# Optimization experiments

Hardware: AMD Instinct MI355X
Metric: run time of the kernel (lower is better)

## Reference

```python
import jax, jax.numpy as jnp
import numpy as np

B, V = 4, 10242
N = B * V            # 40968 packed vertices
E_PER = 30720        # edges per mesh
HID = 128


def _bilinear_sample(fm, grid):
    """pytorch3d vert_align core: grid_sample(align_corners=True, bilinear).
    fm: [B,C,H,W], grid: [B,V,2] xy in [-1,1] -> [B,V,C]."""
    b_, c_, h_, w_ = fm.shape
    x = (grid[..., 0] + 1.0) * 0.5 * (w_ - 1)
    y = (grid[..., 1] + 1.0) * 0.5 * (h_ - 1)
    x0f, y0f = jnp.floor(x), jnp.floor(y)
    wx1, wy1 = x - x0f, y - y0f
    wx0, wy0 = 1.0 - wx1, 1.0 - wy1
    x0 = jnp.clip(x0f, 0, w_ - 1).astype(jnp.int32)
    x1 = jnp.clip(x0f + 1, 0, w_ - 1).astype(jnp.int32)
    y0 = jnp.clip(y0f, 0, h_ - 1).astype(jnp.int32)
    y1 = jnp.clip(y0f + 1, 0, h_ - 1).astype(jnp.int32)
    fmt = jnp.transpose(fm, (0, 2, 3, 1))  # [B,H,W,C]
    bi = jnp.arange(b_)[:, None]
    g = lambda yy, xx: fmt[bi, yy, xx]     # [B,V,C]
    return ((wy0 * wx0)[..., None] * g(y0, x0)
            + (wy0 * wx1)[..., None] * g(y0, x1)
            + (wy1 * wx0)[..., None] * g(y1, x0)
            + (wy1 * wx1)[..., None] * g(y1, x1))


def _graph_conv(x, edges, w0, b0, w1, b1):
    """pytorch3d GraphConv (undirected): W0 x_i + sum over both edge dirs of W1 x_j."""
    h0 = x @ w0 + b0
    h1 = x @ w1 + b1
    e0, e1 = edges[:, 0], edges[:, 1]
    agg = jnp.zeros_like(h0).at[e0].add(h1[e1]).at[e1].add(h1[e0])
    return h0 + agg


def setup_inputs() -> dict:
    key = jax.random.key(0)
    ks = jax.random.split(key, 20)
    s = 0.05
    # per-mesh edges, offset into packed index space
    e = jax.random.randint(ks[0], (B, E_PER, 2), 0, V)
    e = e + (jnp.arange(B) * V)[:, None, None]
    return {
        "feat1": jax.random.normal(ks[1], (B, 256, 56, 56), jnp.float32),
        "feat2": jax.random.normal(ks[2], (B, 512, 28, 28), jnp.float32),
        "feat3": jax.random.normal(ks[3], (B, 1024, 14, 14), jnp.float32),
        "feat4": jax.random.normal(ks[4], (B, 2048, 7, 7), jnp.float32),
        "aligned_verts": jax.random.uniform(ks[5], (B, V, 3), jnp.float32, -1.0, 1.0),
        "verts_packed": jax.random.normal(ks[6], (N, 3), jnp.float32),
        "image_enc": jax.random.normal(ks[7], (B, 256), jnp.float32),
        "edges": e.reshape(B * E_PER, 2).astype(jnp.int64),
        "bottleneck_w": jax.random.normal(ks[8], (3840, HID), jnp.float32) * s,
        "bottleneck_b": jnp.zeros((HID,), jnp.float32),
        "g0_w0": jax.random.normal(ks[9], (387, HID), jnp.float32) * s,
        "g0_b0": jnp.zeros((HID,), jnp.float32),
        "g0_w1": jax.random.normal(ks[10], (387, HID), jnp.float32) * s,
        "g0_b1": jnp.zeros((HID,), jnp.float32),
        "gw0": jax.random.normal(ks[11], (7, HID, HID), jnp.float32) * s,
        "gb0": jnp.zeros((7, HID), jnp.float32),
        "gw1": jax.random.normal(ks[12], (7, HID, HID), jnp.float32) * s,
        "gb1": jnp.zeros((7, HID), jnp.float32),
        "off_w": jax.random.normal(ks[13], (HID, 3), jnp.float32) * s,
        "off_b": jnp.zeros((3,), jnp.float32),
    }


def reference(feat1, feat2, feat3, feat4, aligned_verts, verts_packed, image_enc,
              edges, bottleneck_w, bottleneck_b, g0_w0, g0_b0, g0_w1, g0_b1,
              gw0, gb0, gw1, gb1, off_w, off_b):
    grid = aligned_verts[..., :2]  # vert_align uses xy only
    samp = jnp.concatenate([_bilinear_sample(f, grid)
                            for f in (feat1, feat2, feat3, feat4)], axis=-1)
    samp = samp.reshape(N, 3840)  # return_packed=True
    vfeat = jax.nn.relu(samp @ bottleneck_w + bottleneck_b)
    enc = jnp.repeat(image_enc, V, axis=0)  # repeat_interleave
    x = jnp.concatenate([vfeat, verts_packed, enc], axis=1)  # [N,387]
    x = jax.nn.relu(_graph_conv(x, edges, g0_w0, g0_b0, g0_w1, g0_b1))
    for i in range(7):
        x = jax.nn.relu(_graph_conv(x, edges, gw0[i], gb0[i], gw1[i], gb1[i]))
    return x @ off_w + off_b  # delta_v [N,3]
```

## Files before the change

### kernel.cpp

```cpp
#include <hip/hip_runtime.h>

static inline int ceil_div(int a, int b) { return (a + b - 1) / b; }

typedef __attribute__((ext_vector_type(8))) short short8;
typedef __attribute__((ext_vector_type(4))) float floatx4;

__device__ __forceinline__ unsigned short f2bf(float f) {
    unsigned int u = __float_as_uint(f);
    unsigned int r = (u + 0x7fffu + ((u >> 16) & 1u)) >> 16;
    return (unsigned short)r;
}
__device__ __forceinline__ float bf2f(unsigned short h) {
    return __uint_as_float(((unsigned int)h) << 16);
}

__global__ __launch_bounds__(1024) void scan1_k(const int* __restrict__ deg,
                                                int* __restrict__ excl,
                                                int* __restrict__ bsum, int Nv) {
    __shared__ int s[1024];
    int tid = threadIdx.x;
    int i = blockIdx.x * 1024 + tid;
    int v = (i < Nv) ? deg[i] : 0;
    s[tid] = v;
    __syncthreads();
    for (int off = 1; off < 1024; off <<= 1) {
        int t = (tid >= off) ? s[tid - off] : 0;
        __syncthreads();
        if (tid >= off) s[tid] += t;
        __syncthreads();
    }
    if (i < Nv) excl[i] = s[tid] - v;
    if (tid == 1023) bsum[blockIdx.x] = s[1023];
}

__global__ __launch_bounds__(64) void scan2_k(int* __restrict__ bsum, int nb) {
    __shared__ int s[64];
    int tid = threadIdx.x;
    int v = (tid < nb) ? bsum[tid] : 0;
    s[tid] = v;
    __syncthreads();
    for (int off = 1; off < 64; off <<= 1) {
        int t = (tid >= off) ? s[tid - off] : 0;
        __syncthreads();
        if (tid >= off) s[tid] += t;
        __syncthreads();
    }
    if (tid < nb) bsum[tid] = s[tid] - v;
}

__global__ __launch_bounds__(1024) void scan3_k(const int* __restrict__ excl,
                                                const int* __restrict__ bsum,
                                                const int* __restrict__ deg,
                                                int* __restrict__ rowptr,
                                                int* __restrict__ cursor, int Nv) {
    int i = blockIdx.x * 1024 + threadIdx.x;
    if (i < Nv) {
        int val = excl[i] + bsum[blockIdx.x];
        rowptr[i] = val;
        cursor[i] = val;
        if (i == Nv - 1) rowptr[Nv] = val + deg[i];
    }
}

__global__ __launch_bounds__(256) void fill_adj_k(const int* __restrict__ edges,
                                                  int* __restrict__ cursor,
                                                  int* __restrict__ adj, int E) {
    int e = blockIdx.x * blockDim.x + threadIdx.x;
    if (e < E) {
        int a = edges[2 * e], b = edges[2 * e + 1];
        adj[atomicAdd(&cursor[a], 1)] = b;
        adj[atomicAdd(&cursor[b], 1)] = a;
    }
}

__global__ __launch_bounds__(256) void fatpre_k(const int* __restrict__ edges,
                                                int* __restrict__ deg, int E, int nE,
                                                const float* __restrict__ g0w0,
                                                const float* __restrict__ g0w1,
                                                const float* __restrict__ gw0,
                                                const float* __restrict__ gw1,
                                                unsigned short* __restrict__ Wt,
                                                const float* __restrict__ bw,
                                                unsigned short* __restrict__ bwT,
                                                const float* __restrict__ enc,
                                                float* __restrict__ encp, int B_) {
    int bid = blockIdx.x;
    int tid = threadIdx.x;
    if (bid < nE) {
        int e = bid * 256 + tid;
        if (e < E) {
            atomicAdd(&deg[edges[2 * e]], 1);
            atomicAdd(&deg[edges[2 * e + 1]], 1);
        }
    } else if (bid < nE + 16) {
        int lh = bid - nE;
        int l = lh >> 1, h = lh & 1;
        const float* src;
        if (l == 0) src = h ? g0w1 : g0w0;
        else src = (h ? gw1 : gw0) + (size_t)(l - 1) * 16384;
        unsigned short* dst = Wt + (size_t)lh * 16384;
        for (int idx = tid; idx < 16384; idx += 256) {
            int n = idx >> 7, k = idx & 127;
            dst[n * 128 + k] = f2bf(src[k * 128 + n]);
        }
    } else if (bid < nE + 46) {
        int blk = bid - nE - 16;
        for (int idx = tid; idx < 16384; idx += 256) {
            int n = idx >> 7, kk = idx & 127;
            bwT[(size_t)n * 3840 + blk * 128 + kk] =
                f2bf(bw[(size_t)(blk * 128 + kk) * 128 + n]);
        }
    } else {
        int b = bid - nE - 46;
        int sH = tid >> 7;
        int j = tid & 127;
        const float* w = sH ? g0w1 : g0w0;
        const float* eb = enc + b * 256;
        float acc = 0.f;
        for (int c = 0; c < 256; ++c) acc = fmaf(eb[c], w[(131 + c) * 128 + j], acc);
        encp[(sH * B_ + b) * 128 + j] = acc;
    }
}

__global__ __launch_bounds__(256) void proj_all_k(
    const float* __restrict__ fm1, const float* __restrict__ fm2,
    const float* __restrict__ fm3, const float* __restrict__ fm4,
    const unsigned short* __restrict__ bwT, float* __restrict__ o1, float* __restrict__ o2,
    float* __restrict__ o3, float* __restrict__ o4, int B_) {
    __shared__ unsigned short wlds[8192];

    int tid = threadIdx.x;
    int n1 = 49 * B_ * 2, n2 = 13 * B_ * 4, n3 = 4 * B_ * 8;
    int bid = blockIdx.x;
    const float* fm;
    float* op;
    int C, HW, PT, idx, koff;
    if (bid < n1) {
        fm = fm1; op = o1; C = 256; HW = 3136; PT = 49; idx = bid; koff = 0;
    } else if (bid < n1 + n2) {
        fm = fm2; op = o2; C = 512; HW = 784; PT = 13; idx = bid - n1; koff = 256;
    } else if (bid < n1 + n2 + n3) {
        fm = fm3; op = o3; C = 1024; HW = 196; PT = 4; idx = bid - n1 - n2; koff = 768;
    } else {
        fm = fm4; op = o4; C = 2048; HW = 49; PT = 1; idx = bid - n1 - n2 - n3; koff = 1792;
    }
    int pt = idx % PT;
    int r2 = idx / PT;
    int b = r2 % B_;
    int zz = r2 / B_;
    int p0 = pt * 64;
    const float* fmb = fm + (size_t)b * C * HW;
    int kcf0 = zz * 128;

    int wave = tid >> 6, lane = tid & 63;
    int row16 = lane & 15, quad = lane >> 4;
    int p = p0 + wave * 16 + row16;
    bool pok = (p < HW);
    int pc = pok ? p : 0;

    floatx4 acc[8];
#pragma unroll
    for (int j = 0; j < 8; ++j) acc[j] = (floatx4){0.f, 0.f, 0.f, 0.f};

#pragma unroll
    for (int zz2 = 0; zz2 < 2; ++zz2) {
        int kcf = kcf0 + zz2 * 64;
        int kcw = koff + kcf;
        if (zz2) __syncthreads();
#pragma unroll
        for (int l = 0; l < 4; ++l) {
            int i2 = tid + l * 256;
            int n = i2 >> 3, c16 = i2 & 7;
            *(short8*)&wlds[n * 64 + ((c16 ^ (n & 7)) * 8)] =
                *(const short8*)(bwT + (size_t)n * 3840 + kcw + c16 * 8);
        }
        short8 ax[2];
#pragma unroll
        for (int ks = 0; ks < 2; ++ks) {
#pragma unroll
            for (int j = 0; j < 8; ++j) {
                float v = pok ? fmb[(size_t)(kcf + ks * 32 + quad * 8 + j) * HW + pc] : 0.f;
                ax[ks][j] = (short)f2bf(v);
            }
        }
        __syncthreads();
#pragma unroll
        for (int ks = 0; ks < 2; ++ks) {
            int c = ks * 4 + quad;
#pragma unroll
            for (int nt = 0; nt < 8; ++nt) {
                int wr = nt * 16 + row16;
                short8 bwf = *(short8*)&wlds[wr * 64 + ((c ^ (wr & 7)) * 8)];
                acc[nt] =
                    __builtin_amdgcn_mfma_f32_16x16x32_bf16(ax[ks], bwf, acc[nt], 0, 0, 0);
            }
        }
    }

    float* obase = op + (size_t)b * HW * 128;
#pragma unroll
    for (int nt = 0; nt < 8; ++nt) {
        int colg = nt * 16 + row16;
#pragma unroll
        for (int rr = 0; rr < 4; ++rr) {
            int pr = p0 + wave * 16 + quad * 4 + rr;
            if (pr < HW) atomicAdd(&obase[(size_t)pr * 128 + colg], acc[nt][rr]);
        }
    }
}

__device__ __forceinline__ float sample_level(const float* __restrict__ pp, int Hh, int Ww,
                                              float gx, float gy, int j) {
    float x = (gx + 1.f) * 0.5f * (float)(Ww - 1);
    float y = (gy + 1.f) * 0.5f * (float)(Hh - 1);
    float x0f = floorf(x), y0f = floorf(y);
    float wx1 = x - x0f, wy1 = y - y0f;
    float wx0 = 1.f - wx1, wy0 = 1.f - wy1;
    int x0 = (int)fminf(fmaxf(x0f, 0.f), (float)(Ww - 1));
    int x1 = (int)fminf(fmaxf(x0f + 1.f, 0.f), (float)(Ww - 1));
    int y0 = (int)fminf(fmaxf(y0f, 0.f), (float)(Hh - 1));
    int y1 = (int)fminf(fmaxf(y0f + 1.f, 0.f), (float)(Hh - 1));
    const float* r00 = pp + (size_t)(y0 * Ww + x0) * 128;
    const float* r01 = pp + (size_t)(y0 * Ww + x1) * 128;
    const float* r10 = pp + (size_t)(y1 * Ww + x0) * 128;
    const float* r11 = pp + (size_t)(y1 * Ww + x1) * 128;
    return wy0 * (wx0 * r00[j] + wx1 * r01[j]) + wy1 * (wx0 * r10[j] + wx1 * r11[j]);
}

__global__ __launch_bounds__(128) void sample_bottleneck_k(
    const float* __restrict__ av, const float* __restrict__ pp1, const float* __restrict__ pp2,
    const float* __restrict__ pp3, const float* __restrict__ pp4, const float* __restrict__ bb,
    const float* __restrict__ verts, const float* __restrict__ encp,
    const float* __restrict__ g0w0, const float* __restrict__ g0w1,
    const float* __restrict__ g0b0, const float* __restrict__ g0b1,
    unsigned short* __restrict__ X, unsigned short* __restrict__ H, int V_, int B_) {
    int n = blockIdx.x, j = threadIdx.x;
    int b = n / V_;
    float gx = av[(size_t)n * 3 + 0];
    float gy = av[(size_t)n * 3 + 1];
    float acc = bb[j];
    acc += sample_level(pp1 + (size_t)b * 3136 * 128, 56, 56, gx, gy, j);
    acc += sample_level(pp2 + (size_t)b * 784 * 128, 28, 28, gx, gy, j);
    acc += sample_level(pp3 + (size_t)b * 196 * 128, 14, 14, gx, gy, j);
    acc += sample_level(pp4 + (size_t)b * 49 * 128, 7, 7, gx, gy, j);
    X[(size_t)n * 128 + j] = f2bf(fmaxf(acc, 0.f));
    float v0 = verts[n * 3 + 0], v1 = verts[n * 3 + 1], v2 = verts[n * 3 + 2];
    float h0 = encp[(0 * B_ + b) * 128 + j] + g0b0[j] + v0 * g0w0[128 * 128 + j] +
               v1 * g0w0[129 * 128 + j] + v2 * g0w0[130 * 128 + j];
    float h1 = encp[(1 * B_ + b) * 128 + j] + g0b1[j] + v0 * g0w1[128 * 128 + j] +
               v1 * g0w1[129 * 128 + j] + v2 * g0w1[130 * 128 + j];
    H[(size_t)n * 256 + j] = f2bf(h0);
    H[(size_t)n * 256 + 128 + j] = f2bf(h1);
}

__global__ __launch_bounds__(256) void agg0_k(const unsigned short* __restrict__ X,
                                              const unsigned short* __restrict__ H,
                                              const int* __restrict__ rowptr,
                                              const int* __restrict__ adj,
                                              unsigned short* __restrict__ AggX,
                                              unsigned short* __restrict__ AggH, int Nv) {
    int wave = threadIdx.x >> 6, lane = threadIdx.x & 63;
    int n0 = (blockIdx.x * 4 + wave) * 2;
    if (n0 >= Nv) return;
    const unsigned int* Xu = (const unsigned int*)X;
    int r0 = rowptr[n0], r1 = rowptr[n0 + 1], r2 = rowptr[n0 + 2];
    float a0 = 0.f, a1 = 0.f, b0 = 0.f, b1 = 0.f;
    float c0 = 0.f, c1 = 0.f, d0 = 0.f, d1 = 0.f;
    int tA = r0, tB = r1;
    while (tA < r1 || tB < r2) {
        int nbA[8], nbB[8];
        unsigned int wA[8], wB[8], hA[8], hB[8];
#pragma unroll
        for (int q = 0; q < 8; ++q) {
            int ia = tA + q; ia = (ia < r1) ? ia : (r1 - 1); ia = (ia < 0) ? 0 : ia;
            nbA[q] = adj[ia];
            int ib = tB + q; ib = (ib < r2) ? ib : (r2 - 1); ib = (ib < 0) ? 0 : ib;
            nbB[q] = adj[ib];
        }
#pragma unroll
        for (int q = 0; q < 8; ++q) {
            wA[q] = Xu[(size_t)nbA[q] * 64 + lane];
            wB[q] = Xu[(size_t)nbB[q] * 64 + lane];
            hA[q] = *(const unsigned int*)(H + (size_t)nbA[q] * 256 + 128 + 2 * lane);
            hB[q] = *(const unsigned int*)(H + (size_t)nbB[q] * 256 + 128 + 2 * lane);
        }
#pragma unroll
        for (int q = 0; q < 8; ++q) {
            if (tA + q < r1) {
                a0 += bf2f((unsigned short)(wA[q] & 0xffff));
                a1 += bf2f((unsigned short)(wA[q] >> 16));
                c0 += bf2f((unsigned short)(hA[q] & 0xffff));
                c1 += bf2f((unsigned short)(hA[q] >> 16));
            }
            if (tB + q < r2) {
                b0 += bf2f((unsigned short)(wB[q] & 0xffff));
                b1 += bf2f((unsigned short)(wB[q] >> 16));
                d0 += bf2f((unsigned short)(hB[q] & 0xffff));
                d1 += bf2f((unsigned short)(hB[q] >> 16));
            }
        }
        tA += 8;
        tB += 8;
    }
    *(unsigned int*)(AggX + (size_t)n0 * 128 + 2 * lane) =
        (unsigned int)f2bf(a0) | ((unsigned int)f2bf(a1) << 16);
    *(unsigned int*)(AggX + (size_t)(n0 + 1) * 128 + 2 * lane) =
        (unsigned int)f2bf(b0) | ((unsigned int)f2bf(b1) << 16);
    *(unsigned int*)(AggH + (size_t)n0 * 128 + 2 * lane) =
        (unsigned int)f2bf(c0) | ((unsigned int)f2bf(c1) << 16);
    *(unsigned int*)(AggH + (size_t)(n0 + 1) * 128 + 2 * lane) =
        (unsigned int)f2bf(d0) | ((unsigned int)f2bf(d1) << 16);
}

__global__ __launch_bounds__(256) void agg_x_k(const unsigned short* __restrict__ X,
                                               const int* __restrict__ rowptr,
                                               const int* __restrict__ adj,
                                               unsigned short* __restrict__ Agg, int Nv,
                                               int Etot) {
    int wave = threadIdx.x >> 6, lane = threadIdx.x & 63;
    int n0 = (blockIdx.x * 4 + wave) * 4;
    if (n0 >= Nv) return;
    int g = lane >> 4, c = lane & 15;
    int rp = rowptr[min(n0 + (lane & 7), Nv)];
    int sg = __shfl(rp, g);
    int eg = __shfl(rp, g + 1);
    int m = eg - sg;
    m = max(m, __shfl_xor(m, 16));
    m = max(m, __shfl_xor(m, 32));

    float acc[8];
#pragma unroll
    for (int j = 0; j < 8; ++j) acc[j] = 0.f;

    for (int it = 0; it < m; it += 8) {
        int t = sg + it + (lane & 7);
        int adjv = adj[min(t, Etot - 1)];
        short8 buf[8];
#pragma unroll
        for (int q = 0; q < 8; ++q) {
            int nbq = __shfl(adjv, (lane & 48) + q);
            buf[q] = *(const short8*)(X + (size_t)nbq * 128 + c * 8);
        }
#pragma unroll
        for (int q = 0; q < 8; ++q) {
            bool ok = (sg + it + q < eg);
#pragma unroll
            for (int j = 0; j < 8; ++j) {
                float v = bf2f((unsigned short)buf[q][j]);
                acc[j] += ok ? v : 0.f;
            }
        }
    }

    if (n0 + g < Nv) {
        short8 o;
#pragma unroll
        for (int j = 0; j < 8; ++j) o[j] = (short)f2bf(acc[j]);
        *(short8*)(Agg + (size_t)(n0 + g) * 128 + c * 8) = o;
    }
}

__global__ __launch_bounds__(256, 3) void gemm_dual_k(
    const unsigned short* __restrict__ Xin, const unsigned short* __restrict__ Agg,
    const unsigned short* __restrict__ Wt,
    const float* __restrict__ b0, const float* __restrict__ b1,
    const unsigned short* __restrict__ h0b, const unsigned short* __restrict__ aggh,
    const int* __restrict__ degv, unsigned short* __restrict__ Xout, int M) {
    __shared__ unsigned short wlds[16384];
    __shared__ unsigned short cs[64 * 72];
    __shared__ float bS[128];

    int tid = threadIdx.x;
    int m0 = blockIdx.x * 128;
    int yb = blockIdx.y;

    int wave = tid >> 6, lane = tid & 63;
    int row16 = lane & 15;
    int quad = lane >> 4;
    int wrow = wave * 16;

    short8 axT[2][4], agT[2][4];
    int dgT[2][4];
    {
        int g = min(m0 + wrow + row16, M - 1);
#pragma unroll
        for (int ks = 0; ks < 4; ++ks) {
            int koff = ks * 32 + quad * 8;
            axT[0][ks] = *(const short8*)(Xin + (size_t)g * 128 + koff);
            agT[0][ks] = *(const short8*)(Agg + (size_t)g * 128 + koff);
        }
#pragma unroll
        for (int rr = 0; rr < 4; ++rr)
            dgT[0][rr] = degv[min(m0 + wrow + quad * 4 + rr, M - 1)];
    }

    if (tid < 64) {
        bS[tid] = b0 ? b0[yb * 64 + tid] : 0.f;
        bS[64 + tid] = b1 ? b1[yb * 64 + tid] : 0.f;
    }

    const unsigned short* W0h = Wt + (size_t)yb * 64 * 128;
    const unsigned short* W1h = Wt + 16384 + (size_t)yb * 64 * 128;
#pragma unroll
    for (int l = 0; l < 8; ++l) {
        int idx = tid + l * 256;
        int half = idx >> 10;
        int r = (idx >> 4) & 63;
        int c16 = idx & 15;
        int sw = (c16 ^ (r & 15)) * 8;
        const unsigned short* src = (half ? W1h : W0h) + r * 128 + c16 * 8;
        *(short8*)&wlds[half * 8192 + r * 128 + sw] = *(const short8*)src;
    }
    __syncthreads();

    {
        int g = min(m0 + 64 + wrow + row16, M - 1);
#pragma unroll
        for (int ks = 0; ks < 4; ++ks) {
            int koff = ks * 32 + quad * 8;
            axT[1][ks] = *(const short8*)(Xin + (size_t)g * 128 + koff);
            agT[1][ks] = *(const short8*)(Agg + (size_t)g * 128 + koff);
        }
#pragma unroll
        for (int rr = 0; rr < 4; ++rr)
            dgT[1][rr] = degv[min(m0 + 64 + wrow + quad * 4 + rr, M - 1)];
    }

#pragma unroll
    for (int t = 0; t < 2; ++t) {
        int mT = m0 + t * 64;
        floatx4 acc[4];
#pragma unroll
        for (int j = 0; j < 4; j++) acc[j] = (floatx4){0.f, 0.f, 0.f, 0.f};

#pragma unroll
        for (int ks = 0; ks < 4; ++ks) {
            int c = ks * 4 + quad;
#pragma unroll
            for (int nt = 0; nt < 4; ++nt) {
                int wr = nt * 16 + row16;
                short8 bw0 = *(short8*)&wlds[wr * 128 + ((c ^ row16) * 8)];
                short8 bw1 = *(short8*)&wlds[8192 + wr * 128 + ((c ^ row16) * 8)];
                acc[nt] = __builtin_amdgcn_mfma_f32_16x16x32_bf16(axT[t][ks], bw0, acc[nt], 0, 0, 0);
                acc[nt] = __builtin_amdgcn_mfma_f32_16x16x32_bf16(agT[t][ks], bw1, acc[nt], 0, 0, 0);
            }
        }

#pragma unroll
        for (int nt = 0; nt < 4; ++nt) {
            int colh = nt * 16 + row16;
            int colg = yb * 64 + colh;
            float bc0 = bS[colh];
            float bc1 = bS[64 + colh];
#pragma unroll
            for (int rr = 0; rr < 4; ++rr) {
                int row = wrow + quad * 4 + rr;
                int gm = mT + row;
                float v = acc[nt][rr] + bc0 + (float)dgT[t][rr] * bc1;
                if (h0b && gm < M)
                    v += bf2f(h0b[(size_t)gm * 256 + colg]) +
                         bf2f(aggh[(size_t)gm * 128 + colg]);
                cs[row * 72 + colh] = f2bf(fmaxf(v, 0.f));
            }
        }
        __syncthreads();

        {
            int r = tid >> 2;
            int cq = (tid & 3) * 16;
            int gm = mT + r;
            if (gm < M) {
                unsigned short* dst = Xout + (size_t)gm * 128 + yb * 64 + cq;
                *(short8*)dst = *(short8*)&cs[r * 72 + cq];
                *(short8*)(dst + 8) = *(short8*)&cs[r * 72 + cq + 8];
            }
        }
        __syncthreads();
    }
}

__global__ __launch_bounds__(256) void head_k(const unsigned short* __restrict__ X,
                                              const float* __restrict__ off_w,
                                              const float* __restrict__ off_b,
                                              float* __restrict__ out, int Nv) {
    int wave = threadIdx.x >> 6, lane = threadIdx.x & 63;
    int n = blockIdx.x * 4 + wave;
    if (n >= Nv) return;
    unsigned int u = *(const unsigned int*)(X + (size_t)n * 128 + 2 * lane);
    float x0 = bf2f((unsigned short)(u & 0xffff));
    float x1 = bf2f((unsigned short)(u >> 16));
    int c0 = 2 * lane, c1 = 2 * lane + 1;
    float p0 = x0 * off_w[c0 * 3 + 0] + x1 * off_w[c1 * 3 + 0];
    float p1 = x0 * off_w[c0 * 3 + 1] + x1 * off_w[c1 * 3 + 1];
    float p2 = x0 * off_w[c0 * 3 + 2] + x1 * off_w[c1 * 3 + 2];
#pragma unroll
    for (int m = 1; m < 64; m <<= 1) {
        p0 += __shfl_xor(p0, m);
        p1 += __shfl_xor(p1, m);
        p2 += __shfl_xor(p2, m);
    }
    if (lane == 0) {
        out[n * 3 + 0] = p0 + off_b[0];
        out[n * 3 + 1] = p1 + off_b[1];
        out[n * 3 + 2] = p2 + off_b[2];
    }
}

extern "C" void kernel_launch(void* const* d_in, const int* in_sizes, int n_in, void* d_out,
                              int out_size, void* d_ws, size_t ws_size, hipStream_t stream) {
    const float* feat1 = (const float*)d_in[0];
    const float* feat2 = (const float*)d_in[1];
    const float* feat3 = (const float*)d_in[2];
    const float* feat4 = (const float*)d_in[3];
    const float* av = (const float*)d_in[4];
    const float* verts = (const float*)d_in[5];
    const float* image_enc = (const float*)d_in[6];
    const int* edges = (const int*)d_in[7];
    const float* bw = (const float*)d_in[8];
    const float* bb = (const float*)d_in[9];
    const float* g0w0 = (const float*)d_in[10];
    const float* g0b0 = (const float*)d_in[11];
    const float* g0w1 = (const float*)d_in[12];
    const float* g0b1 = (const float*)d_in[13];
    const float* gw0 = (const float*)d_in[14];
    const float* gb0 = (const float*)d_in[15];
    const float* gw1 = (const float*)d_in[16];
    const float* gb1 = (const float*)d_in[17];
    const float* off_w = (const float*)d_in[18];
    const float* off_b = (const float*)d_in[19];

    int B_ = in_sizes[6] / 256;
    int N_ = in_sizes[5] / 3;
    int V_ = N_ / B_;
    int E_ = in_sizes[7] / 2;

    char* wsb = (char*)d_ws;
    size_t off = 0;
    auto alloc = [&](size_t bytes) -> void* {
        void* p = (void*)(wsb + off);
        off += (bytes + 255) & ~(size_t)255;
        return p;
    };
    int S1 = B_ * 3136 * 128;
    int S2 = B_ * 784 * 128;
    int S3 = B_ * 196 * 128;
    int S4 = B_ * 49 * 128;
    float* pp1 = (float*)alloc((size_t)S1 * 4);
    float* pp2 = (float*)alloc((size_t)S2 * 4);
    float* pp3 = (float*)alloc((size_t)S3 * 4);
    float* pp4 = (float*)alloc((size_t)S4 * 4);
    size_t pp_bytes = off;
    unsigned short* XA = (unsigned short*)alloc((size_t)N_ * 128 * 2);
    unsigned short* XB = (unsigned short*)alloc((size_t)N_ * 128 * 2);
    unsigned short* AggB = (unsigned short*)alloc((size_t)N_ * 128 * 2);
    unsigned short* AggH = (unsigned short*)alloc((size_t)N_ * 128 * 2);
    unsigned short* Hb = (unsigned short*)alloc((size_t)N_ * 256 * 2);
    unsigned short* Wt = (unsigned short*)alloc((size_t)8 * 2 * 128 * 128 * 2);
    unsigned short* bwT = (unsigned short*)alloc((size_t)128 * 3840 * 2);
    float* encp = (float*)alloc((size_t)2 * B_ * 128 * 4);
    int* deg = (int*)alloc((size_t)(N_ + 1) * 4);
    int* rowptr = (int*)alloc((size_t)(N_ + 1) * 4);
    int* cursor = (int*)alloc((size_t)N_ * 4);
    int* excl = (int*)alloc((size_t)N_ * 4);
    int* bsum = (int*)alloc((size_t)64 * 4);
    int* adj = (int*)alloc((size_t)2 * E_ * 4);

    hipMemsetAsync(deg, 0, (N_ + 1) * sizeof(int), stream);
    hipMemsetAsync(wsb, 0, pp_bytes, stream);

    int nE = ceil_div(E_, 256);
    fatpre_k<<<nE + 46 + B_, 256, 0, stream>>>(edges, deg, E_, nE, g0w0, g0w1, gw0, gw1, Wt,
                                               bw, bwT, image_enc, encp, B_);

    int nb = ceil_div(N_, 1024);
    scan1_k<<<nb, 1024, 0, stream>>>(deg, excl, bsum, N_);
    scan2_k<<<1, 64, 0, stream>>>(bsum, nb);
    scan3_k<<<nb, 1024, 0, stream>>>(excl, bsum, deg, rowptr, cursor, N_);
    fill_adj_k<<<ceil_div(E_, 256), 256, 0, stream>>>(edges, cursor, adj, E_);

    int nproj = 49 * B_ * 2 + 13 * B_ * 4 + 4 * B_ * 8 + 1 * B_ * 16;
    proj_all_k<<<nproj, 256, 0, stream>>>(feat1, feat2, feat3, feat4, bwT, pp1, pp2, pp3, pp4,
                                          B_);

    sample_bottleneck_k<<<N_, 128, 0, stream>>>(av, pp1, pp2, pp3, pp4, bb, verts, encp, g0w0,
                                                g0w1, g0b0, g0b1, XA, Hb, V_, B_);

    dim3 ggrid(ceil_div(N_, 128), 2);
    agg0_k<<<ceil_div(N_, 8), 256, 0, stream>>>(XA, Hb, rowptr, adj, AggB, AggH, N_);
    gemm_dual_k<<<ggrid, 256, 0, stream>>>(XA, AggB, Wt, nullptr, nullptr, Hb, AggH, deg, XB,
                                           N_);
    unsigned short* Xc = XB;
    unsigned short* Xn = XA;
    int agrid4 = ceil_div(N_, 16);
    for (int i = 0; i < 7; ++i) {
        agg_x_k<<<agrid4, 256, 0, stream>>>(Xc, rowptr, adj, AggB, N_, 2 * E_);
        gemm_dual_k<<<ggrid, 256, 0, stream>>>(Xc, AggB, Wt + (size_t)(i + 1) * 32768,
                                               gb0 + i * 128, gb1 + i * 128, nullptr, nullptr,
                                               deg, Xn, N_);
        unsigned short* t = Xc;
        Xc = Xn;
        Xn = t;
    }
    head_k<<<ceil_div(N_, 4), 256, 0, stream>>>(Xc, off_w, off_b, (float*)d_out, N_);
}
```

Measured before the change: 428.4 us.

## Fuse head into last GEMM, merge scan stages, vectorize layer-0 aggregation

Removes the separate scan2 kernel by having each scan3 block compute its own prefix offset with a wave reduction. Rewrites agg0 to the agg_x layout: four nodes per wave, 16 lanes per node, short8 vector gathers. It also folds the self h0 term into AggH, so the GEMM epilogue no longer reads h0b. The final output head is fused into the last GEMM epilogue using shuffle reductions and atomicAdd into a zeroed output. This saves launches and one activation round-trip, but adds float atomics whose accumulation order is nondeterministic.

After: 431.4 us, median of 2. Within noise of the previous version (+0.7%).

```diff
diff --git a/kernel.cpp b/kernel.cpp
--- a/kernel.cpp
+++ b/kernel.cpp
@@ -33,29 +33,22 @@
     if (tid == 1023) bsum[blockIdx.x] = s[1023];
 }
 
-__global__ __launch_bounds__(64) void scan2_k(int* __restrict__ bsum, int nb) {
-    __shared__ int s[64];
-    int tid = threadIdx.x;
-    int v = (tid < nb) ? bsum[tid] : 0;
-    s[tid] = v;
-    __syncthreads();
-    for (int off = 1; off < 64; off <<= 1) {
-        int t = (tid >= off) ? s[tid - off] : 0;
-        __syncthreads();
-        if (tid >= off) s[tid] += t;
-        __syncthreads();
-    }
-    if (tid < nb) bsum[tid] = s[tid] - v;
-}
-
 __global__ __launch_bounds__(1024) void scan3_k(const int* __restrict__ excl,
                                                 const int* __restrict__ bsum,
                                                 const int* __restrict__ deg,
                                                 int* __restrict__ rowptr,
-                                                int* __restrict__ cursor, int Nv) {
+                                                int* __restrict__ cursor, int Nv, int nb) {
+    __shared__ int offS;
+    if (threadIdx.x < 64) {
+        int v = (threadIdx.x < min((int)blockIdx.x, nb)) ? bsum[threadIdx.x] : 0;
+#pragma unroll
+        for (int m = 1; m < 64; m <<= 1) v += __shfl_xor(v, m);
+        if (threadIdx.x == 0) offS = v;
+    }
+    __syncthreads();
     int i = blockIdx.x * 1024 + threadIdx.x;
     if (i < Nv) {
-        int val = excl[i] + bsum[blockIdx.x];
+        int val = excl[i] + offS;
         rowptr[i] = val;
         cursor[i] = val;
         if (i == Nv - 1) rowptr[Nv] = val + deg[i];
@@ -258,58 +251,60 @@
                                               const int* __restrict__ rowptr,
                                               const int* __restrict__ adj,
                                               unsigned short* __restrict__ AggX,
-                                              unsigned short* __restrict__ AggH, int Nv) {
+                                              unsigned short* __restrict__ AggH, int Nv,
+                                              int Etot) {
     int wave = threadIdx.x >> 6, lane = threadIdx.x & 63;
-    int n0 = (blockIdx.x * 4 + wave) * 2;
+    int n0 = (blockIdx.x * 4 + wave) * 4;
     if (n0 >= Nv) return;
-    const unsigned int* Xu = (const unsigned int*)X;
-    int r0 = rowptr[n0], r1 = rowptr[n0 + 1], r2 = rowptr[n0 + 2];
-    float a0 = 0.f, a1 = 0.f, b0 = 0.f, b1 = 0.f;
-    float c0 = 0.f, c1 = 0.f, d0 = 0.f, d1 = 0.f;
-    int tA = r0, tB = r1;
-    while (tA < r1 || tB < r2) {
-        int nbA[8], nbB[8];
-        unsigned int wA[8], wB[8], hA[8], hB[8];
+    int g = lane >> 4, c = lane & 15;
+    int rp = rowptr[min(n0 + (lane & 7), Nv)];
+    int sg = __shfl(rp, g);
+    int eg = __shfl(rp, g + 1);
+    int m = eg - sg;
+    m = max(m, __shfl_xor(m, 16));
+    m = max(m, __shfl_xor(m, 32));
+
+    int n = n0 + g;
+    bool nok = (n < Nv);
+    int nc = nok ? n : (Nv - 1);
+    float accx[8], acch[8];
+    short8 h0v = *(const short8*)(H + (size_t)nc * 256 + c * 8);
+#pragma unroll
+    for (int j = 0; j < 8; ++j) {
+        accx[j] = 0.f;
+        acch[j] = bf2f((unsigned short)h0v[j]);
+    }
+
+    for (int it = 0; it < m; it += 8) {
+        int t = sg + it + (lane & 7);
+        int adjv = adj[min(t, Etot - 1)];
+        short8 bx[8], bh[8];
 #pragma unroll
         for (int q = 0; q < 8; ++q) {
-            int ia = tA + q; ia = (ia < r1) ? ia : (r1 - 1); ia = (ia < 0) ? 0 : ia;
-            nbA[q] = adj[ia];
-            int ib = tB + q; ib = (ib < r2) ? ib : (r2 - 1); ib = (ib < 0) ? 0 : ib;
-            nbB[q] = adj[ib];
+            int nbq = __shfl(adjv, (lane & 48) + q);
+            bx[q] = *(const short8*)(X + (size_t)nbq * 128 + c * 8);
+            bh[q] = *(const short8*)(H + (size_t)nbq * 256 + 128 + c * 8);
         }
 #pragma unroll
         for (int q = 0; q < 8; ++q) {
-            wA[q] = Xu[(size_t)nbA[q] * 64 + lane];
-            wB[q] = Xu[(size_t)nbB[q] * 64 + lane];
-            hA[q] = *(const unsigned int*)(H + (size_t)nbA[q] * 256 + 128 + 2 * lane);
-            hB[q] = *(const unsigned int*)(H + (size_t)nbB[q] * 256 + 128 + 2 * lane);
-        }
-#pragma unroll
-        for (int q = 0; q < 8; ++q) {
-            if (tA + q < r1) {
-                a0 += bf2f((unsigned short)(wA[q] & 0xffff));
-                a1 += bf2f((unsigned short)(wA[q] >> 16));
-                c0 += bf2f((unsigned short)(hA[q] & 0xffff));
-                c1 += bf2f((unsigned short)(hA[q] >> 16));
-            }
-            if (tB + q < r2) {
-                b0 += bf2f((unsigned short)(wB[q] & 0xffff));
-                b1 += bf2f((unsigned short)(wB[q] >> 16));
-                d0 += bf2f((unsigned short)(hB[q] & 0xffff));
-                d1 += bf2f((unsigned short)(hB[q] >> 16));
-            }
-        }
-        tA += 8;
-        tB += 8;
-    }
-    *(unsigned int*)(AggX + (size_t)n0 * 128 + 2 * lane) =
-        (unsigned int)f2bf(a0) | ((unsigned int)f2bf(a1) << 16);
-    *(unsigned int*)(AggX + (size_t)(n0 + 1) * 128 + 2 * lane) =
-        (unsigned int)f2bf(b0) | ((unsigned int)f2bf(b1) << 16);
-    *(unsigned int*)(AggH + (size_t)n0 * 128 + 2 * lane) =
-        (unsigned int)f2bf(c0) | ((unsigned int)f2bf(c1) << 16);
-    *(unsigned int*)(AggH + (size_t)(n0 + 1) * 128 + 2 * lane) =
-        (unsigned int)f2bf(d0) | ((unsigned int)f2bf(d1) << 16);
+            bool ok = (sg + it + q < eg);
+#pragma unroll
+            for (int j = 0; j < 8; ++j) {
+                accx[j] += ok ? bf2f((unsigned short)bx[q][j]) : 0.f;
+                acch[j] += ok ? bf2f((unsigned short)bh[q][j]) : 0.f;
+            }
+        }
+    }
+    if (nok) {
+        short8 ox, oh;
+#pragma unroll
+        for (int j = 0; j < 8; ++j) {
+            ox[j] = (short)f2bf(accx[j]);
+            oh[j] = (short)f2bf(acch[j]);
+        }
+        *(short8*)(AggX + (size_t)n * 128 + c * 8) = ox;
+        *(short8*)(AggH + (size_t)n * 128 + c * 8) = oh;
+    }
 }
 
 __global__ __launch_bounds__(256) void agg_x_k(const unsigned short* __restrict__ X,
@@ -364,11 +359,13 @@
     const unsigned short* __restrict__ Xin, const unsigned short* __restrict__ Agg,
     const unsigned short* __restrict__ Wt,
     const float* __restrict__ b0, const float* __restrict__ b1,
-    const unsigned short* __restrict__ h0b, const unsigned short* __restrict__ aggh,
-    const int* __restrict__ degv, unsigned short* __restrict__ Xout, int M) {
+    const unsigned short* __restrict__ aggh, const int* __restrict__ degv,
+    unsigned short* __restrict__ Xout, int M, const float* __restrict__ ow,
+    const float* __restrict__ ob, float* __restrict__ outp) {
     __shared__ unsigned short wlds[16384];
     __shared__ unsigned short cs[64 * 72];
     __shared__ float bS[128];
+    __shared__ float owS[192];
 
     int tid = threadIdx.x;
     int m0 = blockIdx.x * 128;
@@ -398,6 +395,7 @@
         bS[tid] = b0 ? b0[yb * 64 + tid] : 0.f;
         bS[64 + tid] = b1 ? b1[yb * 64 + tid] : 0.f;
     }
+    if (outp && tid < 192) owS[tid] = ow[yb * 192 + tid];
 
     const unsigned short* W0h = Wt + (size_t)yb * 64 * 128;
     const unsigned short* W1h = Wt + 16384 + (size_t)yb * 64 * 128;
@@ -446,6 +444,7 @@
             }
         }
 
+        unsigned short cvs[4][4];
 #pragma unroll
         for (int nt = 0; nt < 4; ++nt) {
             int colh = nt * 16 + row16;
@@ -457,10 +456,42 @@
                 int row = wrow + quad * 4 + rr;
                 int gm = mT + row;
                 float v = acc[nt][rr] + bc0 + (float)dgT[t][rr] * bc1;
-                if (h0b && gm < M)
-                    v += bf2f(h0b[(size_t)gm * 256 + colg]) +
-                         bf2f(aggh[(size_t)gm * 128 + colg]);
-                cs[row * 72 + colh] = f2bf(fmaxf(v, 0.f));
+                if (aggh && gm < M) v += bf2f(aggh[(size_t)gm * 128 + colg]);
+                unsigned short cv = f2bf(fmaxf(v, 0.f));
+                cvs[nt][rr] = cv;
+                cs[row * 72 + colh] = cv;
+            }
+        }
+
+        if (outp) {
+#pragma unroll
+            for (int rr = 0; rr < 4; ++rr) {
+                float h0 = 0.f, h1 = 0.f, h2 = 0.f;
+#pragma unroll
+                for (int nt = 0; nt < 4; ++nt) {
+                    int colh = nt * 16 + row16;
+                    float xv = bf2f(cvs[nt][rr]);
+                    h0 += xv * owS[colh * 3 + 0];
+                    h1 += xv * owS[colh * 3 + 1];
+                    h2 += xv * owS[colh * 3 + 2];
+                }
+#pragma unroll
+                for (int mm = 1; mm < 16; mm <<= 1) {
+                    h0 += __shfl_xor(h0, mm);
+                    h1 += __shfl_xor(h1, mm);
+                    h2 += __shfl_xor(h2, mm);
+                }
+                if (row16 == 0) {
+                    int gm = mT + wrow + quad * 4 + rr;
+                    if (gm < M) {
+                        float e0 = (yb == 0) ? ob[0] : 0.f;
+                        float e1 = (yb == 0) ? ob[1] : 0.f;
+                        float e2 = (yb == 0) ? ob[2] : 0.f;
+                        atomicAdd(&outp[gm * 3 + 0], h0 + e0);
+                        atomicAdd(&outp[gm * 3 + 1], h1 + e1);
+                        atomicAdd(&outp[gm * 3 + 2], h2 + e2);
+                    }
+                }
             }
         }
         __syncthreads();
@@ -476,33 +507,6 @@
             }
         }
         __syncthreads();
-    }
-}
-
-__global__ __launch_bounds__(256) void head_k(const unsigned short* __restrict__ X,
-                                              const float* __restrict__ off_w,
-                                              const float* __restrict__ off_b,
-                                              float* __restrict__ out, int Nv) {
-    int wave = threadIdx.x >> 6, lane = threadIdx.x & 63;
-    int n = blockIdx.x * 4 + wave;
-    if (n >= Nv) return;
-    unsigned int u = *(const unsigned int*)(X + (size_t)n * 128 + 2 * lane);
-    float x0 = bf2f((unsigned short)(u & 0xffff));
-    float x1 = bf2f((unsigned short)(u >> 16));
-    int c0 = 2 * lane, c1 = 2 * lane + 1;
-    float p0 = x0 * off_w[c0 * 3 + 0] + x1 * off_w[c1 * 3 + 0];
-    float p1 = x0 * off_w[c0 * 3 + 1] + x1 * off_w[c1 * 3 + 1];
-    float p2 = x0 * off_w[c0 * 3 + 2] + x1 * off_w[c1 * 3 + 2];
-#pragma unroll
-    for (int m = 1; m < 64; m <<= 1) {
-        p0 += __shfl_xor(p0, m);
-        p1 += __shfl_xor(p1, m);
-        p2 += __shfl_xor(p2, m);
-    }
-    if (lane == 0) {
-        out[n * 3 + 0] = p0 + off_b[0];
-        out[n * 3 + 1] = p1 + off_b[1];
-        out[n * 3 + 2] = p2 + off_b[2];
     }
 }
 
@@ -567,6 +571,7 @@
 
     hipMemsetAsync(deg, 0, (N_ + 1) * sizeof(int), stream);
     hipMemsetAsync(wsb, 0, pp_bytes, stream);
+    hipMemsetAsync(d_out, 0, out_size, stream);
 
     int nE = ceil_div(E_, 256);
     fatpre_k<<<nE + 46 + B_, 256, 0, stream>>>(edges, deg, E_, nE, g0w0, g0w1, gw0, gw1, Wt,
@@ -574,8 +579,7 @@
 
     int nb = ceil_div(N_, 1024);
     scan1_k<<<nb, 1024, 0, stream>>>(deg, excl, bsum, N_);
-    scan2_k<<<1, 64, 0, stream>>>(bsum, nb);
-    scan3_k<<<nb, 1024, 0, stream>>>(excl, bsum, deg, rowptr, cursor, N_);
+    scan3_k<<<nb, 1024, 0, stream>>>(excl, bsum, deg, rowptr, cursor, N_, nb);
     fill_adj_k<<<ceil_div(E_, 256), 256, 0, stream>>>(edges, cursor, adj, E_);
 
     int nproj = 49 * B_ * 2 + 13 * B_ * 4 + 4 * B_ * 8 + 1 * B_ * 16;
@@ -586,20 +590,22 @@
                                                 g0w1, g0b0, g0b1, XA, Hb, V_, B_);
 
     dim3 ggrid(ceil_div(N_, 128), 2);
-    agg0_k<<<ceil_div(N_, 8), 256, 0, stream>>>(XA, Hb, rowptr, adj, AggB, AggH, N_);
-    gemm_dual_k<<<ggrid, 256, 0, stream>>>(XA, AggB, Wt, nullptr, nullptr, Hb, AggH, deg, XB,
-                                           N_);
+    int agrid4 = ceil_div(N_, 16);
+    agg0_k<<<agrid4, 256, 0, stream>>>(XA, Hb, rowptr, adj, AggB, AggH, N_, 2 * E_);
+    gemm_dual_k<<<ggrid, 256, 0, stream>>>(XA, AggB, Wt, nullptr, nullptr, AggH, deg, XB, N_,
+                                           nullptr, nullptr, nullptr);
     unsigned short* Xc = XB;
     unsigned short* Xn = XA;
-    int agrid4 = ceil_div(N_, 16);
     for (int i = 0; i < 7; ++i) {
+        bool last = (i == 6);
         agg_x_k<<<agrid4, 256, 0, stream>>>(Xc, rowptr, adj, AggB, N_, 2 * E_);
         gemm_dual_k<<<ggrid, 256, 0, stream>>>(Xc, AggB, Wt + (size_t)(i + 1) * 32768,
-                                               gb0 + i * 128, gb1 + i * 128, nullptr, nullptr,
-                                               deg, Xn, N_);
+                                               gb0 + i * 128, gb1 + i * 128, nullptr, deg, Xn,
+                                               N_, last ? off_w : nullptr,
+                                               last ? off_b : nullptr,
+                                               last ? (float*)d_out : nullptr);
         unsigned short* t = Xc;
         Xc = Xn;
         Xn = t;
     }
-    head_k<<<ceil_div(N_, 4), 256, 0, stream>>>(Xc, off_w, off_b, (float*)d_out, N_);
-}
+}
```
